# Performance work log

Hardware: AMD Instinct MI355X
Metric: run time of the kernel (lower is better)

Reference implementation:

```python
import jax, jax.numpy as jnp
import numpy as np


def _slice_coeffs(grid, guide):
    """Trilinear slice of bilateral grid at (x, y, guide) per full-res pixel.
    grid:  [B, C, D, Hg, Wg]  (C=12 affine coeffs)
    guide: [B, 1, H, W] in [0, 1]
    returns coeffs [B, C, H, W]
    """
    B, C, D, Hg, Wg = grid.shape
    H, W = guide.shape[2], guide.shape[3]
    g = guide[:, 0]  # [B, H, W]

    # HDRNet sampling convention: pixel centers mapped into grid coords
    gx = (jnp.arange(W, dtype=grid.dtype) + 0.5) / W * Wg - 0.5   # [W]
    gy = (jnp.arange(H, dtype=grid.dtype) + 0.5) / H * Hg - 0.5   # [H]
    gz = g * D - 0.5                                              # [B, H, W]

    gx = jnp.broadcast_to(gx[None, None, :], (B, H, W))
    gy = jnp.broadcast_to(gy[None, :, None], (B, H, W))

    fx0 = jnp.floor(gx); fy0 = jnp.floor(gy); fz0 = jnp.floor(gz)
    wx = gx - fx0; wy = gy - fy0; wz = gz - fz0  # trilinear fractions

    x0 = jnp.clip(fx0.astype(jnp.int32), 0, Wg - 1)
    x1 = jnp.clip(fx0.astype(jnp.int32) + 1, 0, Wg - 1)
    y0 = jnp.clip(fy0.astype(jnp.int32), 0, Hg - 1)
    y1 = jnp.clip(fy0.astype(jnp.int32) + 1, 0, Hg - 1)
    z0 = jnp.clip(fz0.astype(jnp.int32), 0, D - 1)
    z1 = jnp.clip(fz0.astype(jnp.int32) + 1, 0, D - 1)

    def gather_one(gb, zi, yi, xi):
        # gb: [C, D, Hg, Wg]; zi/yi/xi: [H, W] -> [C, H, W]
        return gb[:, zi, yi, xi]

    gather = jax.vmap(gather_one)  # over batch

    out = jnp.zeros((B, C, H, W), dtype=grid.dtype)
    for zi, wzc in ((z0, 1.0 - wz), (z1, wz)):
        for yi, wyc in ((y0, 1.0 - wy), (y1, wy)):
            for xi, wxc in ((x0, 1.0 - wx), (x1, wx)):
                w = (wzc * wyc * wxc)[:, None]  # [B, 1, H, W]
                out = out + w * gather(grid, zi, yi, xi)
    return out


def setup_inputs() -> dict:
    key = jax.random.key(0)
    k1, k2, k3 = jax.random.split(key, 3)
    Bilterial_Grid = jax.random.normal(k1, (4, 12, 8, 16, 16), dtype=jnp.float32)
    Guide = jax.random.uniform(k2, (4, 1, 1024, 1024), dtype=jnp.float32)
    fr = jax.random.uniform(k3, (4, 3, 1024, 1024), dtype=jnp.float32)
    return {"Bilterial_Grid": Bilterial_Grid, "Guide": Guide, "fr": fr}


def reference(Bilterial_Grid, Guide, fr):
    B, _, H, W = fr.shape
    coeffs = _slice_coeffs(Bilterial_Grid, Guide)          # [B, 12, H, W]
    co = coeffs.reshape(B, 3, 4, H, W)                      # 3x4 affine per pixel
    # out_c = sum_i A[c,i] * fr_i + b[c]
    out = jnp.einsum('boihw,bihw->bohw', co[:, :, :3], fr) + co[:, :, 3]
    return out
```

## Files before the change

kernel.cpp:

```cpp
#include <hip/hip_runtime.h>


#define SSTRIDE 116

__global__ __launch_bounds__(256, 3) void slice_apply_f32(
    const float* __restrict__ grid,
    const float* __restrict__ guide,
    const float* __restrict__ fr,
    float* __restrict__ out)
{
    __shared__ float lds[8 * SSTRIDE];

    const int b     = blockIdx.y;
    const int tileX = blockIdx.x & 15;
    const int tileY = blockIdx.x >> 4;
    const int t     = threadIdx.x;

    int px[3], py[3];
#pragma unroll
    for (int j = 0; j < 3; ++j) {
        px[j] = min(max(tileX - 1 + j, 0), 15);
        py[j] = min(max(tileY - 1 + j, 0), 15);
    }

    for (int e = t; e < 8 * 9 * 12; e += 256) {
        const int c    = e % 12;
        const int cell = (e / 12) % 9;
        const int s    = e / 108;
        lds[s * SSTRIDE + cell * 12 + c] =
            grid[((b * 12 + c) * 8 + s) * 256 + py[cell / 3] * 16 + px[cell % 3]];
    }
    __syncthreads();

    const int lx4 = (t & 15) * 4;
    const int r   = t >> 4;
    const int bx  = (lx4 >= 32) ? 1 : 0;

    const int y0p = tileY << 6;
    const int x0p = tileX << 6;

#pragma unroll
    for (int it = 0; it < 4; ++it) {
        const int ly = (it << 4) + r;
        const int y  = y0p + ly;
        const int by = it >> 1;
        const float wy = (ly + 0.5f) * 0.015625f + (0.5f - (float)by);
        const float v1 = wy, v0 = 1.0f - wy;

        const int gofs = (b * 1024 + y) * 1024 + x0p + lx4;
        const int fofs = ((b * 3) * 1024 + y) * 1024 + x0p + lx4;

        const float4 gv  = *reinterpret_cast<const float4*>(guide + gofs);
        const float4 f0v = *reinterpret_cast<const float4*>(fr + fofs);
        const float4 f1v = *reinterpret_cast<const float4*>(fr + fofs + 1048576);
        const float4 f2v = *reinterpret_cast<const float4*>(fr + fofs + 2097152);

        const float gva[4] = {gv.x, gv.y, gv.z, gv.w};
        const float fa0[4] = {f0v.x, f0v.y, f0v.z, f0v.w};
        const float fa1[4] = {f1v.x, f1v.y, f1v.z, f1v.w};
        const float fa2[4] = {f2v.x, f2v.y, f2v.z, f2v.w};

        float o0a[4], o1a[4], o2a[4];

#pragma unroll
        for (int p = 0; p < 4; ++p) {
            const float g  = gva[p];
            const float gz = g * 8.0f - 0.5f;
            int s = (int)floorf(gz);
            s = min(max(s, 0), 7);
            const float wz = fmaxf(gz - (float)s, 0.0f);
            const int s2 = min(s + 1, 7);
            const float zl = 1.0f - wz, zh = wz;

            const float wx = (float)(lx4 + p) * 0.015625f +
                             (0.0078125f + 0.5f - (float)bx);
            const float u1 = wx, u0 = 1.0f - wx;

            float acc[12];
#pragma unroll
            for (int c = 0; c < 12; ++c) acc[c] = 0.0f;

            const int bA = s * SSTRIDE, bB = s2 * SSTRIDE;
#pragma unroll
            for (int dy = 0; dy < 2; ++dy) {
#pragma unroll
                for (int dx = 0; dx < 2; ++dx) {
                    const int co = ((by + dy) * 3 + (bx + dx)) * 12;
                    const float w  = (dy ? v1 : v0) * (dx ? u1 : u0);
                    const float wl = w * zl;
                    const float wh = w * zh;
                    const float4* pA = reinterpret_cast<const float4*>(&lds[bA + co]);
                    const float4* pB = reinterpret_cast<const float4*>(&lds[bB + co]);
#pragma unroll
                    for (int q = 0; q < 3; ++q) {
                        const float4 a  = pA[q];
                        const float4 bb = pB[q];
                        acc[q * 4 + 0] = fmaf(wl, a.x, acc[q * 4 + 0]);
                        acc[q * 4 + 0] = fmaf(wh, bb.x, acc[q * 4 + 0]);
                        acc[q * 4 + 1] = fmaf(wl, a.y, acc[q * 4 + 1]);
                        acc[q * 4 + 1] = fmaf(wh, bb.y, acc[q * 4 + 1]);
                        acc[q * 4 + 2] = fmaf(wl, a.z, acc[q * 4 + 2]);
                        acc[q * 4 + 2] = fmaf(wh, bb.z, acc[q * 4 + 2]);
                        acc[q * 4 + 3] = fmaf(wl, a.w, acc[q * 4 + 3]);
                        acc[q * 4 + 3] = fmaf(wh, bb.w, acc[q * 4 + 3]);
                    }
                }
            }

            const float f0 = fa0[p], f1 = fa1[p], f2 = fa2[p];
            o0a[p] = fmaf(acc[0], f0, fmaf(acc[1], f1, fmaf(acc[2],  f2, acc[3])));
            o1a[p] = fmaf(acc[4], f0, fmaf(acc[5], f1, fmaf(acc[6],  f2, acc[7])));
            o2a[p] = fmaf(acc[8], f0, fmaf(acc[9], f1, fmaf(acc[10], f2, acc[11])));
        }

        const float4 O0 = {o0a[0], o0a[1], o0a[2], o0a[3]};
        const float4 O1 = {o1a[0], o1a[1], o1a[2], o1a[3]};
        const float4 O2 = {o2a[0], o2a[1], o2a[2], o2a[3]};
        *reinterpret_cast<float4*>(out + fofs)           = O0;
        *reinterpret_cast<float4*>(out + fofs + 1048576) = O1;
        *reinterpret_cast<float4*>(out + fofs + 2097152) = O2;
    }
}

extern "C" void kernel_launch(void* const* d_in, const int* in_sizes, int n_in,
                              void* d_out, int out_size, void* d_ws, size_t ws_size,
                              hipStream_t stream) {
    const float* grid  = (const float*)d_in[0];
    const float* guide = (const float*)d_in[1];
    const float* fr    = (const float*)d_in[2];
    float* out = (float*)d_out;

    dim3 g(256, 4);
    dim3 blk(256);
    hipLaunchKernelGGL(slice_apply_f32, g, blk, 0, stream, grid, guide, fr, out);
}
```

Measured before the change: 127.4 us.

## Pack z-adjacent grid coefficients as bf16 pairs in LDS and remap warps to quadrants

Grid coefficients are stored in LDS as bf16 pairs, with slice s and s+1 packed into one 32-bit word, so each pixel's trilinear gather reads half as much LDS (one uint4 per quad instead of two float4). Each wavefront now covers one 32x32 quadrant, which makes the bx/by cell offsets uniform per wave. The x weights are precomputed per thread and the launch-bounds occupancy hint goes from 3 to 4. Rounding the coefficients to bf16 adds precision loss that may exceed the fp32 tolerance.

```diff
diff --git a/kernel.cpp b/kernel.cpp
--- a/kernel.cpp
+++ b/kernel.cpp
@@ -1,15 +1,27 @@
 #include <hip/hip_runtime.h>
 
 
-#define SSTRIDE 116
+#define ZSTRIDE 132
 
-__global__ __launch_bounds__(256, 3) void slice_apply_f32(
+static __device__ __forceinline__ unsigned short f2bf(float f) {
+    unsigned int u = __float_as_uint(f);
+    u += ((u >> 16) & 1u) + 0x7FFFu;
+    return (unsigned short)(u >> 16);
+}
+static __device__ __forceinline__ float bf_lo(unsigned int d) {
+    return __uint_as_float(d << 16);
+}
+static __device__ __forceinline__ float bf_hi(unsigned int d) {
+    return __uint_as_float(d & 0xFFFF0000u);
+}
+
+__global__ __launch_bounds__(256, 4) void slice_apply(
     const float* __restrict__ grid,
     const float* __restrict__ guide,
     const float* __restrict__ fr,
     float* __restrict__ out)
 {
-    __shared__ float lds[8 * SSTRIDE];
+    __shared__ unsigned int lds[8 * ZSTRIDE];
 
     const int b     = blockIdx.y;
     const int tileX = blockIdx.x & 15;
@@ -27,28 +39,47 @@
         const int c    = e % 12;
         const int cell = (e / 12) % 9;
         const int s    = e / 108;
-        lds[s * SSTRIDE + cell * 12 + c] =
-            grid[((b * 12 + c) * 8 + s) * 256 + py[cell / 3] * 16 + px[cell % 3]];
+        const int s2   = min(s + 1, 7);
+        const int cb   = (b * 12 + c) * 8;
+        const int sp   = py[cell / 3] * 16 + px[cell % 3];
+        const float lo = grid[(cb + s)  * 256 + sp];
+        const float hi = grid[(cb + s2) * 256 + sp];
+        lds[s * ZSTRIDE + cell * 12 + c] =
+            (unsigned int)f2bf(lo) | ((unsigned int)f2bf(hi) << 16);
     }
     __syncthreads();
 
-    const int lx4 = (t & 15) * 4;
-    const int r   = t >> 4;
-    const int bx  = (lx4 >= 32) ? 1 : 0;
+    const int w  = t >> 6;
+    const int l  = t & 63;
+    const int by = w >> 1;
+    const int bx = w & 1;
+    const int lx = bx * 32 + (l & 7) * 4;
+    const int rr = l >> 3;
 
-    const int y0p = tileY << 6;
-    const int x0p = tileX << 6;
+    float u0[4], u1[4];
+#pragma unroll
+    for (int p = 0; p < 4; ++p) {
+        const float wx = ((float)(lx + p) + 0.5f) * 0.015625f + (0.5f - (float)bx);
+        u1[p] = wx;
+        u0[p] = 1.0f - wx;
+    }
+
+    int cofs[4];
+#pragma unroll
+    for (int k = 0; k < 4; ++k) {
+        const int dy = k >> 1, dx = k & 1;
+        cofs[k] = ((by + dy) * 3 + (bx + dx)) * 12;
+    }
 
 #pragma unroll
     for (int it = 0; it < 4; ++it) {
-        const int ly = (it << 4) + r;
-        const int y  = y0p + ly;
-        const int by = it >> 1;
-        const float wy = (ly + 0.5f) * 0.015625f + (0.5f - (float)by);
+        const int ly = by * 32 + it * 8 + rr;
+        const int y  = tileY * 64 + ly;
+        const float wy = ((float)ly + 0.5f) * 0.015625f + (0.5f - (float)by);
         const float v1 = wy, v0 = 1.0f - wy;
 
-        const int gofs = (b * 1024 + y) * 1024 + x0p + lx4;
-        const int fofs = ((b * 3) * 1024 + y) * 1024 + x0p + lx4;
+        const int gofs = (b * 1024 + y) * 1024 + tileX * 64 + lx;
+        const int fofs = ((b * 3) * 1024 + y) * 1024 + tileX * 64 + lx;
 
         const float4 gv  = *reinterpret_cast<const float4*>(guide + gofs);
         const float4 f0v = *reinterpret_cast<const float4*>(fr + fofs);
@@ -69,40 +100,28 @@
             int s = (int)floorf(gz);
             s = min(max(s, 0), 7);
             const float wz = fmaxf(gz - (float)s, 0.0f);
-            const int s2 = min(s + 1, 7);
             const float zl = 1.0f - wz, zh = wz;
-
-            const float wx = (float)(lx4 + p) * 0.015625f +
-                             (0.0078125f + 0.5f - (float)bx);
-            const float u1 = wx, u0 = 1.0f - wx;
+            const int sbase = s * ZSTRIDE;
 
             float acc[12];
 #pragma unroll
             for (int c = 0; c < 12; ++c) acc[c] = 0.0f;
 
-            const int bA = s * SSTRIDE, bB = s2 * SSTRIDE;
 #pragma unroll
-            for (int dy = 0; dy < 2; ++dy) {
+            for (int k = 0; k < 4; ++k) {
+                const float wgt = ((k >> 1) ? v1 : v0) * ((k & 1) ? u1[p] : u0[p]);
+                const float wl = wgt * zl;
+                const float wh = wgt * zh;
+                const unsigned int* cp = &lds[sbase + cofs[k]];
 #pragma unroll
-                for (int dx = 0; dx < 2; ++dx) {
-                    const int co = ((by + dy) * 3 + (bx + dx)) * 12;
-                    const float w  = (dy ? v1 : v0) * (dx ? u1 : u0);
-                    const float wl = w * zl;
-                    const float wh = w * zh;
-                    const float4* pA = reinterpret_cast<const float4*>(&lds[bA + co]);
-                    const float4* pB = reinterpret_cast<const float4*>(&lds[bB + co]);
+                for (int q = 0; q < 3; ++q) {
+                    const uint4 dq = *reinterpret_cast<const uint4*>(cp + q * 4);
+                    const unsigned int dw[4] = {dq.x, dq.y, dq.z, dq.w};
 #pragma unroll
-                    for (int q = 0; q < 3; ++q) {
-                        const float4 a  = pA[q];
-                        const float4 bb = pB[q];
-                        acc[q * 4 + 0] = fmaf(wl, a.x, acc[q * 4 + 0]);
-                        acc[q * 4 + 0] = fmaf(wh, bb.x, acc[q * 4 + 0]);
-                        acc[q * 4 + 1] = fmaf(wl, a.y, acc[q * 4 + 1]);
-                        acc[q * 4 + 1] = fmaf(wh, bb.y, acc[q * 4 + 1]);
-                        acc[q * 4 + 2] = fmaf(wl, a.z, acc[q * 4 + 2]);
-                        acc[q * 4 + 2] = fmaf(wh, bb.z, acc[q * 4 + 2]);
-                        acc[q * 4 + 3] = fmaf(wl, a.w, acc[q * 4 + 3]);
-                        acc[q * 4 + 3] = fmaf(wh, bb.w, acc[q * 4 + 3]);
+                    for (int kk = 0; kk < 4; ++kk) {
+                        const int c = q * 4 + kk;
+                        acc[c] = fmaf(wl, bf_lo(dw[kk]), acc[c]);
+                        acc[c] = fmaf(wh, bf_hi(dw[kk]), acc[c]);
                     }
                 }
             }
@@ -132,5 +151,5 @@
 
     dim3 g(256, 4);
     dim3 blk(256);
-    hipLaunchKernelGGL(slice_apply_f32, g, blk, 0, stream, grid, guide, fr, out);
+    hipLaunchKernelGGL(slice_apply, g, blk, 0, stream, grid, guide, fr, out);
 }
```

After: 368.4 us. 2.89x slower.
